# Performance work log

Measured on AMD Instinct MI355X. Metric: run time of the kernel, lower is better.

Reference implementation:

```python
import jax, jax.numpy as jnp
import numpy as np

B, N, D = 16, 1024, 5
R_HID = 8  # radial MLP hidden width


def setup_inputs() -> dict:
    key = jax.random.key(0)
    ks = jax.random.split(key, 16)
    feats = jax.random.normal(ks[0], (B, N, D), jnp.float32)
    coors = 3.0 * jax.random.normal(ks[1], (B, N, 3), jnp.float32)
    a = jax.random.bernoulli(ks[2], 0.01, (B, N, N))
    adj_mat = a | jnp.swapaxes(a, 1, 2)
    s = 1.0 / np.sqrt(D)
    Wq = s * jax.random.normal(ks[3], (D, D), jnp.float32)
    Wk = s * jax.random.normal(ks[4], (D, D), jnp.float32)
    Wv = s * jax.random.normal(ks[5], (D, D), jnp.float32)
    Wo = s * jax.random.normal(ks[6], (D, D), jnp.float32)
    w_r1 = 0.5 * jax.random.normal(ks[7], (1, R_HID), jnp.float32)
    b_r1 = jnp.zeros((R_HID,), jnp.float32)
    w_r2 = 0.5 * jax.random.normal(ks[8], (R_HID, 1), jnp.float32)
    b_r2 = jnp.zeros((1,), jnp.float32)
    w1 = (1.0 / np.sqrt(D)) * jax.random.normal(ks[9], (D, 128), jnp.float32)
    b1 = jnp.zeros((128,), jnp.float32)
    w2 = (1.0 / np.sqrt(128.0)) * jax.random.normal(ks[10], (128, 3), jnp.float32)
    b2 = jnp.zeros((3,), jnp.float32)
    return dict(feats=feats, coors=coors, adj_mat=adj_mat, Wq=Wq, Wk=Wk, Wv=Wv,
                Wo=Wo, w_r1=w_r1, b_r1=b_r1, w_r2=w_r2, b_r2=b_r2,
                w1=w1, b1=b1, w2=w2, b2=b2)


def _se3_layer(feats, coors, neigh, Wq, Wk, Wv, Wo, w_r1, b_r1, w_r2, b_r2):
    # SE(3)-invariant sparse graph attention on degree-0 channels.
    # Attention logits = content term + radial (distance-only) bias, so the
    # scalar output is invariant to global rotations/translations of coors.
    q = jnp.einsum('bnd,de->bne', feats, Wq)
    k = jnp.einsum('bnd,de->bne', feats, Wk)
    v = jnp.einsum('bnd,de->bne', feats, Wv)
    rel = coors[:, :, None, :] - coors[:, None, :, :]        # [B,N,N,3]
    dist = jnp.sqrt(jnp.sum(rel * rel, axis=-1) + 1e-8)      # [B,N,N]
    h = jax.nn.relu(dist[..., None] * w_r1[0] + b_r1)        # [B,N,N,R_HID]
    rbias = (h @ w_r2)[..., 0] + b_r2[0]                     # [B,N,N]
    scores = jnp.einsum('bid,bjd->bij', q, k) / np.sqrt(q.shape[-1]) + rbias
    scores = jnp.where(neigh, scores, -1e9)
    attn = jax.nn.softmax(scores, axis=-1)
    agg = jnp.einsum('bij,bjd->bid', attn, v)
    return feats + jnp.einsum('bid,de->bie', agg, Wo)        # residual


def reference(feats, coors, adj_mat, Wq, Wk, Wv, Wo, w_r1, b_r1, w_r2, b_r2,
              w1, b1, w2, b2):
    a = adj_mat.astype(jnp.float32)
    # num_adj_degrees=2: attend over 1-hop and 2-hop neighbors (+ self)
    adj2 = jnp.einsum('bij,bjk->bik', a, a) > 0
    eye = jnp.eye(adj_mat.shape[1], dtype=bool)[None]
    neigh = adj_mat | adj2 | eye
    x = _se3_layer(feats, coors, neigh, Wq, Wk, Wv, Wo, w_r1, b_r1, w_r2, b_r2)
    pooled = jnp.mean(x, axis=1)                              # [B, D]
    hdn = jax.nn.relu(pooled @ w1 + b1)
    return hdn @ w2 + b2                                      # [B, 3]
```

## Files before the change

kernel.cpp:

```cpp
#include <hip/hip_runtime.h>
#include <hip/hip_bf16.h>

#define BB 16
#define NN 1024
#define DD 5
#define RH 8

typedef unsigned long long u64;
typedef unsigned int u32;
typedef __hip_bfloat16 bf16;

static __device__ __forceinline__ float tof(bf16 x) { return __bfloat162float(x); }
static __device__ __forceinline__ float ldf(const void* p, long long i, bool f) {
  return f ? ((const float*)p)[i] : tof(((const bf16*)p)[i]);
}

__global__ __launch_bounds__(256) void k_pack(const void* __restrict__ adj,
                                              u64* __restrict__ adjbits) {
  __shared__ int sNon01, sNonpair, sLow3;
  int tid = threadIdx.x;
  if (tid == 0) { sNon01 = 0; sNonpair = 0; sLow3 = 0; }
  __syncthreads();
  {
    const u32* aw = (const u32*)adj;
    int non01 = 0, nonpair = 0, low3 = 0;
    for (int i = tid; i < 4096; i += 256) {
      u32 x = aw[i];
      u32 lo = x & 0xFFFFu, hi = x >> 16;
      non01 |= (x > 1u);
      nonpair |= !((lo == 0u || lo == 0x3F80u) && (hi == 0u || hi == 0x3F80u));
      low3 |= (lo == 0x3F80u);
    }
    if (non01) atomicOr(&sNon01, 1);
    if (nonpair) atomicOr(&sNonpair, 1);
    if (low3) atomicOr(&sLow3, 1);
  }
  __syncthreads();
  int mode;
  if (!sNon01) mode = 0;
  else if (!sNonpair) mode = sLow3 ? 2 : 3;
  else mode = 1;

  int gid = blockIdx.x * 256 + tid;
  if (gid >= BB * NN * 16) return;
  int w = gid & 15;
  long long row = gid >> 4;
  long long base = row * NN + (long long)w * 64;
  u64 bits = 0;
  if (mode == 3) {
    const uint4* p = (const uint4*)((const float*)adj + base);
    #pragma unroll
    for (int t = 0; t < 16; ++t) {
      uint4 x = p[t];
      if (x.x << 1) bits |= 1ull << (4 * t + 0);
      if (x.y << 1) bits |= 1ull << (4 * t + 1);
      if (x.z << 1) bits |= 1ull << (4 * t + 2);
      if (x.w << 1) bits |= 1ull << (4 * t + 3);
    }
  } else if (mode == 0) {
    const uint4* p = (const uint4*)((const u32*)adj + base);
    #pragma unroll
    for (int t = 0; t < 16; ++t) {
      uint4 x = p[t];
      if (x.x) bits |= 1ull << (4 * t + 0);
      if (x.y) bits |= 1ull << (4 * t + 1);
      if (x.z) bits |= 1ull << (4 * t + 2);
      if (x.w) bits |= 1ull << (4 * t + 3);
    }
  } else if (mode == 2) {
    const uint4* p = (const uint4*)((const unsigned short*)adj + base);
    #pragma unroll
    for (int t = 0; t < 8; ++t) {
      uint4 x = p[t];
      u32 c[4] = {x.x, x.y, x.z, x.w};
      #pragma unroll
      for (int q = 0; q < 4; ++q) {
        if ((c[q] & 0x7FFFu)) bits |= 1ull << (8 * t + 2 * q + 0);
        if ((c[q] >> 16) & 0x7FFFu) bits |= 1ull << (8 * t + 2 * q + 1);
      }
    }
  } else {
    const uint4* p = (const uint4*)((const unsigned char*)adj + base);
    #pragma unroll
    for (int t = 0; t < 4; ++t) {
      uint4 x = p[t];
      u32 c[4] = {x.x, x.y, x.z, x.w};
      #pragma unroll
      for (int q = 0; q < 4; ++q)
        #pragma unroll
        for (int bb = 0; bb < 4; ++bb)
          if ((c[q] >> (8 * bb)) & 0xFFu) bits |= 1ull << (16 * t + 4 * q + bb);
    }
  }
  adjbits[gid] = bits;
}

__global__ __launch_bounds__(256) void k_twohop(const u64* __restrict__ adjbits,
                                                u64* __restrict__ neighbits) {
  __shared__ unsigned short listL[4][NN];
  int wave = threadIdx.x >> 6, lane = threadIdx.x & 63;
  int row = blockIdx.x * 4 + wave;
  int b = row >> 10;
  int i = row & (NN - 1);
  int w = lane & 15;
  const u64* rowp = adjbits + (size_t)row * 16;
  u64 rw = rowp[w];
  unsigned short* list = listL[wave];
  int cnt = 0;
  #pragma unroll
  for (int sw = 0; sw < 16; ++sw) {
    u64 bits = __shfl(rw, sw, 64);
    int mybit = (int)((bits >> lane) & 1ull);
    int pre = __popcll(bits & ((1ull << lane) - 1ull));
    if (mybit) list[cnt + pre] = (unsigned short)(sw * 64 + lane);
    cnt += __popcll(bits);
  }
  __syncthreads();
  u64 acc = rw;
  if (w == (i >> 6)) acc |= 1ull << (i & 63);
  int g = lane >> 4;
  const u64* basep = adjbits + (size_t)b * NN * 16;
  for (int n = g; n < cnt; n += 4) {
    int j = list[n];
    acc |= basep[(size_t)j * 16 + w];
  }
  acc |= __shfl_xor(acc, 16, 64);
  acc |= __shfl_xor(acc, 32, 64);
  if (lane < 16) neighbits[(size_t)row * 16 + lane] = acc;
}

__global__ __launch_bounds__(256) void k_attn(
    const void* __restrict__ feats, const void* __restrict__ coors,
    const void* __restrict__ Wq, const void* __restrict__ Wk,
    const void* __restrict__ Wv, const void* __restrict__ Wo,
    const void* __restrict__ wr1, const void* __restrict__ br1,
    const void* __restrict__ wr2, const void* __restrict__ br2,
    const u64* __restrict__ neighbits, float* __restrict__ rowAgg) {
  __shared__ __align__(16) float4 kvL[512 * 3];
  __shared__ float coL[512 * 3];
  __shared__ float wqL[25], wkL[25], wvL[25], woL[25];
  __shared__ float qL[16 * DD], ciL[16 * 3];
  __shared__ float wrL[3][RH];
  __shared__ float sConst[2];
  __shared__ int sFast;
  __shared__ int sCnt[4];
  int bi = blockIdx.x;
  int b = bi >> 7, rem = bi & 127, chunk = rem >> 1, half = rem & 1;
  int j0 = half * 512;
  int tid = threadIdx.x;
  {
    u32 x = ((const u32*)feats)[tid];
    u32 lo = x & 0xFFFFu;
    int e = (int)((lo >> 7) & 0xFFu);
    bool insane = !(lo == 0u || (e >= 90 && e <= 150));
    u64 m = __ballot(insane);
    if ((tid & 63) == 0) sCnt[tid >> 6] = (int)__popcll(m);
  }
  __syncthreads();
  bool f32 = (sCnt[0] + sCnt[1] + sCnt[2] + sCnt[3]) > 64;
  if (tid < 25) {
    wqL[tid] = ldf(Wq, tid, f32);
    wkL[tid] = ldf(Wk, tid, f32);
    wvL[tid] = ldf(Wv, tid, f32);
    woL[tid] = ldf(Wo, tid, f32);
  }
  if (tid >= 64 && tid < 64 + RH) {
    int h = tid - 64;
    wrL[0][h] = ldf(wr1, h, f32);
    wrL[1][h] = ldf(br1, h, f32);
    wrL[2][h] = ldf(wr2, h, f32);
  }
  if (tid == 96) {
    float c = 0.0f;
    int ok = 1;
    #pragma unroll
    for (int h = 0; h < RH; ++h) {
      float w1h = ldf(wr1, h, f32);
      if (ldf(br1, h, f32) != 0.0f) ok = 0;
      if (w1h > 0.0f) c += w1h * ldf(wr2, h, f32);
    }
    sConst[0] = c;
    sConst[1] = ldf(br2, 0, f32);
    sFast = ok;
  }
  __syncthreads();
  for (int n = tid; n < 512; n += 256) {
    long long node = (long long)b * NN + j0 + n;
    float f0 = ldf(feats, node * DD + 0, f32), f1 = ldf(feats, node * DD + 1, f32),
          f2 = ldf(feats, node * DD + 2, f32), f3 = ldf(feats, node * DD + 3, f32),
          f4 = ldf(feats, node * DD + 4, f32);
    float k[DD], tv[DD], v[DD];
    #pragma unroll
    for (int e = 0; e < DD; ++e) {
      k[e] = f0 * wkL[e] + f1 * wkL[5 + e] + f2 * wkL[10 + e] + f3 * wkL[15 + e] +
             f4 * wkL[20 + e];
      tv[e] = f0 * wvL[e] + f1 * wvL[5 + e] + f2 * wvL[10 + e] + f3 * wvL[15 + e] +
              f4 * wvL[20 + e];
    }
    #pragma unroll
    for (int e = 0; e < DD; ++e)
      v[e] = tv[0] * woL[e] + tv[1] * woL[5 + e] + tv[2] * woL[10 + e] +
             tv[3] * woL[15 + e] + tv[4] * woL[20 + e];
    kvL[n * 3 + 0] = make_float4(k[0], k[1], k[2], k[3]);
    kvL[n * 3 + 1] = make_float4(k[4], v[0], v[1], v[2]);
    kvL[n * 3 + 2] = make_float4(v[3], v[4], 0.f, 0.f);
  }
  for (int idx = tid; idx < 512 * 3; idx += 256)
    coL[idx] = ldf(coors, (long long)(b * NN + j0) * 3 + idx, f32);
  if (tid < 16) {
    long long row = (long long)b * NN + chunk * 16 + tid;
    float f0 = ldf(feats, row * DD + 0, f32), f1 = ldf(feats, row * DD + 1, f32),
          f2 = ldf(feats, row * DD + 2, f32), f3 = ldf(feats, row * DD + 3, f32),
          f4 = ldf(feats, row * DD + 4, f32);
    #pragma unroll
    for (int e = 0; e < DD; ++e)
      qL[tid * DD + e] = (f0 * wqL[e] + f1 * wqL[5 + e] + f2 * wqL[10 + e] +
                          f3 * wqL[15 + e] + f4 * wqL[20 + e]) * 0.4472135954999579f;
    #pragma unroll
    for (int c = 0; c < 3; ++c) ciL[tid * 3 + c] = ldf(coors, row * 3 + c, f32);
  }
  __syncthreads();

  int g = tid >> 6, lane = tid & 63;
  int i0 = chunk * 16 + g * 4;
  float q[4][DD], ci[4][3], l[4], A[4][DD];
  #pragma unroll
  for (int r = 0; r < 4; ++r) {
    #pragma unroll
    for (int e = 0; e < DD; ++e) q[r][e] = qL[(g * 4 + r) * DD + e];
    #pragma unroll
    for (int c = 0; c < 3; ++c) ci[r][c] = ciL[(g * 4 + r) * 3 + c];
    l[r] = 0.0f;
    #pragma unroll
    for (int e = 0; e < DD; ++e) A[r][e] = 0.0f;
  }
  const u64* nb = neighbits + ((size_t)(b * NN + i0)) * 16 + half * 8;
  float Cf = sConst[0], br2f = sConst[1];
  int fast = sFast;
  for (int it = 0; it < 8; ++it) {
    int j = it * 64 + lane;
    float4 ka = kvL[j * 3 + 0];
    float4 kb = kvL[j * 3 + 1];
    float4 kc = kvL[j * 3 + 2];
    float jx = coL[j * 3], jy = coL[j * 3 + 1], jz = coL[j * 3 + 2];
    if (fast) {
      #pragma unroll
      for (int r = 0; r < 4; ++r) {
        u64 nw = nb[(size_t)r * 16 + it];
        float cx = jx - ci[r][0], cy = jy - ci[r][1], cz = jz - ci[r][2];
        float dist = sqrtf(fmaf(cx, cx, fmaf(cy, cy, fmaf(cz, cz, 1e-8f))));
        float s = fmaf(q[r][0], ka.x, br2f);
        s = fmaf(q[r][1], ka.y, s);
        s = fmaf(q[r][2], ka.z, s);
        s = fmaf(q[r][3], ka.w, s);
        s = fmaf(q[r][4], kb.x, s);
        s = fmaf(Cf, dist, s);
        s = fminf(s, 85.0f);
        s = ((nw >> lane) & 1ull) ? s : -100.0f;
        float p = __expf(s);
        l[r] += p;
        A[r][0] = fmaf(p, kb.y, A[r][0]);
        A[r][1] = fmaf(p, kb.z, A[r][1]);
        A[r][2] = fmaf(p, kb.w, A[r][2]);
        A[r][3] = fmaf(p, kc.x, A[r][3]);
        A[r][4] = fmaf(p, kc.y, A[r][4]);
      }
    } else {
      #pragma unroll
      for (int r = 0; r < 4; ++r) {
        u64 nw = nb[(size_t)r * 16 + it];
        float cx = jx - ci[r][0], cy = jy - ci[r][1], cz = jz - ci[r][2];
        float dist = sqrtf(fmaf(cx, cx, fmaf(cy, cy, fmaf(cz, cz, 1e-8f))));
        float rb = br2f;
        #pragma unroll
        for (int h = 0; h < RH; ++h)
          rb += fmaxf(dist * wrL[0][h] + wrL[1][h], 0.0f) * wrL[2][h];
        float s = fmaf(q[r][0], ka.x, rb);
        s = fmaf(q[r][1], ka.y, s);
        s = fmaf(q[r][2], ka.z, s);
        s = fmaf(q[r][3], ka.w, s);
        s = fmaf(q[r][4], kb.x, s);
        s = fminf(s, 85.0f);
        s = ((nw >> lane) & 1ull) ? s : -100.0f;
        float p = __expf(s);
        l[r] += p;
        A[r][0] = fmaf(p, kb.y, A[r][0]);
        A[r][1] = fmaf(p, kb.z, A[r][1]);
        A[r][2] = fmaf(p, kb.w, A[r][2]);
        A[r][3] = fmaf(p, kc.x, A[r][3]);
        A[r][4] = fmaf(p, kc.y, A[r][4]);
      }
    }
  }
  #pragma unroll
  for (int msk = 1; msk < 64; msk <<= 1) {
    #pragma unroll
    for (int r = 0; r < 4; ++r) {
      l[r] += __shfl_xor(l[r], msk, 64);
      A[r][0] += __shfl_xor(A[r][0], msk, 64);
      A[r][1] += __shfl_xor(A[r][1], msk, 64);
      A[r][2] += __shfl_xor(A[r][2], msk, 64);
      A[r][3] += __shfl_xor(A[r][3], msk, 64);
      A[r][4] += __shfl_xor(A[r][4], msk, 64);
    }
  }
  if (lane == 0) {
    #pragma unroll
    for (int r = 0; r < 4; ++r) {
      float* o = rowAgg + (((size_t)(b * NN + i0 + r)) * 2 + half) * 6;
      o[0] = l[r];
      o[1] = A[r][0]; o[2] = A[r][1]; o[3] = A[r][2]; o[4] = A[r][3]; o[5] = A[r][4];
    }
  }
}

__global__ __launch_bounds__(256) void k_final(
    const void* __restrict__ feats, const float* __restrict__ rowAgg,
    const void* __restrict__ w1, const void* __restrict__ b1,
    const void* __restrict__ w2, const void* __restrict__ b2,
    float* __restrict__ out) {
  __shared__ float waveL[4][DD];
  __shared__ float poolL[DD];
  __shared__ float hL[128];
  __shared__ int sCnt[4];
  int b = blockIdx.x, tid = threadIdx.x;
  {
    u32 x = ((const u32*)feats)[tid];
    u32 lo = x & 0xFFFFu;
    int e = (int)((lo >> 7) & 0xFFu);
    bool insane = !(lo == 0u || (e >= 90 && e <= 150));
    u64 m = __ballot(insane);
    if ((tid & 63) == 0) sCnt[tid >> 6] = (int)__popcll(m);
  }
  __syncthreads();
  bool f32 = (sCnt[0] + sCnt[1] + sCnt[2] + sCnt[3]) > 64;
  float pe[DD] = {0.f, 0.f, 0.f, 0.f, 0.f};
  for (int n = tid; n < NN; n += 256) {
    const float* ag = rowAgg + ((size_t)(b * NN + n)) * 12;
    float l = ag[0] + ag[6];
    float inv = (l > 0.f) ? 1.0f / l : 0.0f;
    long long base = ((long long)b * NN + n) * DD;
    #pragma unroll
    for (int e = 0; e < DD; ++e)
      pe[e] += ldf(feats, base + e, f32) + (ag[1 + e] + ag[7 + e]) * inv;
  }
  #pragma unroll
  for (int off = 32; off >= 1; off >>= 1)
    #pragma unroll
    for (int e = 0; e < DD; ++e) pe[e] += __shfl_down(pe[e], off, 64);
  int wave = tid >> 6, lane = tid & 63;
  if (lane == 0)
    #pragma unroll
    for (int e = 0; e < DD; ++e) waveL[wave][e] = pe[e];
  __syncthreads();
  if (tid < DD)
    poolL[tid] = (waveL[0][tid] + waveL[1][tid] + waveL[2][tid] + waveL[3][tid]) *
                 (1.0f / 1024.0f);
  __syncthreads();
  if (tid < 128) {
    float acc = ldf(b1, tid, f32);
    #pragma unroll
    for (int d = 0; d < DD; ++d)
      acc = fmaf(poolL[d], ldf(w1, d * 128 + tid, f32), acc);
    hL[tid] = fmaxf(acc, 0.0f);
  }
  __syncthreads();
  if (tid < 3) {
    float s = ldf(b2, tid, f32);
    for (int j = 0; j < 128; ++j) s = fmaf(hL[j], ldf(w2, j * 3 + tid, f32), s);
    out[b * 3 + tid] = s;
  }
}

extern "C" void kernel_launch(void* const* d_in, const int* in_sizes, int n_in,
                              void* d_out, int out_size, void* d_ws, size_t ws_size,
                              hipStream_t stream) {
  const void* adj = d_in[2];
  float* out = (float*)d_out;

  char* w = (char*)d_ws;
  const size_t BITS_BYTES = (size_t)BB * NN * 16 * sizeof(u64);
  u64* adjbits = (u64*)(w + 512);
  u64* neighbits = (u64*)(w + 512 + BITS_BYTES);
  float* rowAgg = (float*)(w + 512 + 2 * BITS_BYTES);

  k_pack<<<BB * NN * 16 / 256, 256, 0, stream>>>(adj, adjbits);
  k_twohop<<<BB * NN / 4, 256, 0, stream>>>(adjbits, neighbits);
  k_attn<<<BB * 128, 256, 0, stream>>>(d_in[0], d_in[1], d_in[3], d_in[4], d_in[5],
                                       d_in[6], d_in[7], d_in[8], d_in[9], d_in[10],
                                       neighbits, rowAgg);
  k_final<<<BB, 256, 0, stream>>>(d_in[0], rowAgg, d_in[11], d_in[12],
                                  d_in[13], d_in[14], out);
}
```

Baseline: 202.2 us.

## Fuse final pooling/MLP into attention kernel via atomics and last-block reduction

The attention kernel now processes both halves of the key range in one block (two phases), which halves the grid and removes the rowAgg round-trip. Per-row results are normalized in-kernel and atomically accumulated into a pooled buffer. The last block, found with a done counter, runs the small MLP, which removes the separate k_final launch. The neighbor masks are preloaded into 16-bit registers per row, and the fast path uses exp2 with log2e prescaling plus the hardware sqrt intrinsic. The risks are atomic nondeterminism and the serial last-block tail.

New measurement: 312.1 us. +54.3%, slower.

```diff
diff --git a/kernel.cpp b/kernel.cpp
--- a/kernel.cpp
+++ b/kernel.cpp
@@ -15,10 +15,18 @@
   return f ? ((const float*)p)[i] : tof(((const bf16*)p)[i]);
 }
 
+#define LOG2E 1.4426950408889634f
+
 __global__ __launch_bounds__(256) void k_pack(const void* __restrict__ adj,
-                                              u64* __restrict__ adjbits) {
+                                              u64* __restrict__ adjbits,
+                                              float* __restrict__ pooled,
+                                              int* __restrict__ doneCnt) {
   __shared__ int sNon01, sNonpair, sLow3;
   int tid = threadIdx.x;
+  if (blockIdx.x == 0) {
+    if (tid < BB * DD) pooled[tid] = 0.0f;
+    if (tid == 0) *doneCnt = 0;
+  }
   if (tid == 0) { sNon01 = 0; sNonpair = 0; sLow3 = 0; }
   __syncthreads();
   {
@@ -135,18 +143,20 @@
     const void* __restrict__ Wv, const void* __restrict__ Wo,
     const void* __restrict__ wr1, const void* __restrict__ br1,
     const void* __restrict__ wr2, const void* __restrict__ br2,
-    const u64* __restrict__ neighbits, float* __restrict__ rowAgg) {
+    const u64* __restrict__ neighbits, float* __restrict__ pooled,
+    int* __restrict__ doneCnt,
+    const void* __restrict__ w1v, const void* __restrict__ b1v,
+    const void* __restrict__ w2v, const void* __restrict__ b2v,
+    float* __restrict__ out) {
   __shared__ __align__(16) float4 kvL[512 * 3];
   __shared__ float coL[512 * 3];
   __shared__ float wqL[25], wkL[25], wvL[25], woL[25];
   __shared__ float qL[16 * DD], ciL[16 * 3];
   __shared__ float wrL[3][RH];
   __shared__ float sConst[2];
-  __shared__ int sFast;
+  __shared__ int sFast, sDone;
   __shared__ int sCnt[4];
-  int bi = blockIdx.x;
-  int b = bi >> 7, rem = bi & 127, chunk = rem >> 1, half = rem & 1;
-  int j0 = half * 512;
+  int b = blockIdx.x >> 6, chunk = blockIdx.x & 63;
   int tid = threadIdx.x;
   {
     u32 x = ((const u32*)feats)[tid];
@@ -179,196 +189,202 @@
       if (ldf(br1, h, f32) != 0.0f) ok = 0;
       if (w1h > 0.0f) c += w1h * ldf(wr2, h, f32);
     }
-    sConst[0] = c;
-    sConst[1] = ldf(br2, 0, f32);
+    sConst[0] = c * LOG2E;
+    sConst[1] = ldf(br2, 0, f32) * LOG2E;
     sFast = ok;
   }
   __syncthreads();
-  for (int n = tid; n < 512; n += 256) {
-    long long node = (long long)b * NN + j0 + n;
-    float f0 = ldf(feats, node * DD + 0, f32), f1 = ldf(feats, node * DD + 1, f32),
-          f2 = ldf(feats, node * DD + 2, f32), f3 = ldf(feats, node * DD + 3, f32),
-          f4 = ldf(feats, node * DD + 4, f32);
-    float k[DD], tv[DD], v[DD];
-    #pragma unroll
-    for (int e = 0; e < DD; ++e) {
-      k[e] = f0 * wkL[e] + f1 * wkL[5 + e] + f2 * wkL[10 + e] + f3 * wkL[15 + e] +
-             f4 * wkL[20 + e];
-      tv[e] = f0 * wvL[e] + f1 * wvL[5 + e] + f2 * wvL[10 + e] + f3 * wvL[15 + e] +
-              f4 * wvL[20 + e];
-    }
-    #pragma unroll
-    for (int e = 0; e < DD; ++e)
-      v[e] = tv[0] * woL[e] + tv[1] * woL[5 + e] + tv[2] * woL[10 + e] +
-             tv[3] * woL[15 + e] + tv[4] * woL[20 + e];
-    kvL[n * 3 + 0] = make_float4(k[0], k[1], k[2], k[3]);
-    kvL[n * 3 + 1] = make_float4(k[4], v[0], v[1], v[2]);
-    kvL[n * 3 + 2] = make_float4(v[3], v[4], 0.f, 0.f);
-  }
-  for (int idx = tid; idx < 512 * 3; idx += 256)
-    coL[idx] = ldf(coors, (long long)(b * NN + j0) * 3 + idx, f32);
+  int fast = sFast;
   if (tid < 16) {
     long long row = (long long)b * NN + chunk * 16 + tid;
     float f0 = ldf(feats, row * DD + 0, f32), f1 = ldf(feats, row * DD + 1, f32),
           f2 = ldf(feats, row * DD + 2, f32), f3 = ldf(feats, row * DD + 3, f32),
           f4 = ldf(feats, row * DD + 4, f32);
+    float qsc = fast ? (0.4472135954999579f * LOG2E) : 0.4472135954999579f;
     #pragma unroll
     for (int e = 0; e < DD; ++e)
       qL[tid * DD + e] = (f0 * wqL[e] + f1 * wqL[5 + e] + f2 * wqL[10 + e] +
-                          f3 * wqL[15 + e] + f4 * wqL[20 + e]) * 0.4472135954999579f;
-    #pragma unroll
-    for (int c = 0; c < 3; ++c) ciL[tid * 3 + c] = ldf(coors, row * 3 + c, f32);
-  }
-  __syncthreads();
+                          f3 * wqL[15 + e] + f4 * wqL[20 + e]) * qsc;
+    #pragma unroll
+    for (int c = 0; c < 3; ++c)
+      ciL[tid * 3 + c] = ldf(coors, row * 3 + c, f32);
+  }
 
   int g = tid >> 6, lane = tid & 63;
   int i0 = chunk * 16 + g * 4;
+  u32 msk[4];
+  {
+    const u64* nb = neighbits + ((size_t)(b * NN + i0)) * 16;
+    #pragma unroll
+    for (int r = 0; r < 4; ++r) {
+      u32 mk = 0;
+      #pragma unroll
+      for (int w16 = 0; w16 < 16; ++w16) {
+        u64 word = nb[(size_t)r * 16 + w16];
+        mk |= (u32)((word >> lane) & 1ull) << w16;
+      }
+      msk[r] = mk;
+    }
+  }
   float q[4][DD], ci[4][3], l[4], A[4][DD];
+  float Cf = sConst[0], br2f = sConst[1];
   #pragma unroll
   for (int r = 0; r < 4; ++r) {
-    #pragma unroll
-    for (int e = 0; e < DD; ++e) q[r][e] = qL[(g * 4 + r) * DD + e];
-    #pragma unroll
-    for (int c = 0; c < 3; ++c) ci[r][c] = ciL[(g * 4 + r) * 3 + c];
     l[r] = 0.0f;
     #pragma unroll
     for (int e = 0; e < DD; ++e) A[r][e] = 0.0f;
   }
-  const u64* nb = neighbits + ((size_t)(b * NN + i0)) * 16 + half * 8;
-  float Cf = sConst[0], br2f = sConst[1];
-  int fast = sFast;
-  for (int it = 0; it < 8; ++it) {
-    int j = it * 64 + lane;
-    float4 ka = kvL[j * 3 + 0];
-    float4 kb = kvL[j * 3 + 1];
-    float4 kc = kvL[j * 3 + 2];
-    float jx = coL[j * 3], jy = coL[j * 3 + 1], jz = coL[j * 3 + 2];
-    if (fast) {
+
+  for (int ph = 0; ph < 2; ++ph) {
+    __syncthreads();
+    for (int n = tid; n < 512; n += 256) {
+      long long node = (long long)b * NN + ph * 512 + n;
+      float f0 = ldf(feats, node * DD + 0, f32), f1 = ldf(feats, node * DD + 1, f32),
+            f2 = ldf(feats, node * DD + 2, f32), f3 = ldf(feats, node * DD + 3, f32),
+            f4 = ldf(feats, node * DD + 4, f32);
+      float k[DD], tv[DD], v[DD];
+      #pragma unroll
+      for (int e = 0; e < DD; ++e) {
+        k[e] = f0 * wkL[e] + f1 * wkL[5 + e] + f2 * wkL[10 + e] + f3 * wkL[15 + e] +
+               f4 * wkL[20 + e];
+        tv[e] = f0 * wvL[e] + f1 * wvL[5 + e] + f2 * wvL[10 + e] + f3 * wvL[15 + e] +
+                f4 * wvL[20 + e];
+      }
+      #pragma unroll
+      for (int e = 0; e < DD; ++e)
+        v[e] = tv[0] * woL[e] + tv[1] * woL[5 + e] + tv[2] * woL[10 + e] +
+               tv[3] * woL[15 + e] + tv[4] * woL[20 + e];
+      kvL[n * 3 + 0] = make_float4(k[0], k[1], k[2], k[3]);
+      kvL[n * 3 + 1] = make_float4(k[4], v[0], v[1], v[2]);
+      kvL[n * 3 + 2] = make_float4(v[3], v[4], 0.f, 0.f);
+    }
+    for (int idx = tid; idx < 512 * 3; idx += 256)
+      coL[idx] = ldf(coors, ((long long)(b * NN) + ph * 512) * 3 + idx, f32);
+    __syncthreads();
+    if (ph == 0) {
       #pragma unroll
       for (int r = 0; r < 4; ++r) {
-        u64 nw = nb[(size_t)r * 16 + it];
-        float cx = jx - ci[r][0], cy = jy - ci[r][1], cz = jz - ci[r][2];
-        float dist = sqrtf(fmaf(cx, cx, fmaf(cy, cy, fmaf(cz, cz, 1e-8f))));
-        float s = fmaf(q[r][0], ka.x, br2f);
-        s = fmaf(q[r][1], ka.y, s);
-        s = fmaf(q[r][2], ka.z, s);
-        s = fmaf(q[r][3], ka.w, s);
-        s = fmaf(q[r][4], kb.x, s);
-        s = fmaf(Cf, dist, s);
-        s = fminf(s, 85.0f);
-        s = ((nw >> lane) & 1ull) ? s : -100.0f;
-        float p = __expf(s);
-        l[r] += p;
-        A[r][0] = fmaf(p, kb.y, A[r][0]);
-        A[r][1] = fmaf(p, kb.z, A[r][1]);
-        A[r][2] = fmaf(p, kb.w, A[r][2]);
-        A[r][3] = fmaf(p, kc.x, A[r][3]);
-        A[r][4] = fmaf(p, kc.y, A[r][4]);
+        #pragma unroll
+        for (int e = 0; e < DD; ++e) q[r][e] = qL[(g * 4 + r) * DD + e];
+        #pragma unroll
+        for (int c = 0; c < 3; ++c) ci[r][c] = ciL[(g * 4 + r) * 3 + c];
       }
-    } else {
-      #pragma unroll
-      for (int r = 0; r < 4; ++r) {
-        u64 nw = nb[(size_t)r * 16 + it];
-        float cx = jx - ci[r][0], cy = jy - ci[r][1], cz = jz - ci[r][2];
-        float dist = sqrtf(fmaf(cx, cx, fmaf(cy, cy, fmaf(cz, cz, 1e-8f))));
-        float rb = br2f;
+    }
+    #pragma unroll
+    for (int it = 0; it < 8; ++it) {
+      int itg = ph * 8 + it;
+      int j = it * 64 + lane;
+      float4 ka = kvL[j * 3 + 0];
+      float4 kb = kvL[j * 3 + 1];
+      float4 kc = kvL[j * 3 + 2];
+      float jx = coL[j * 3], jy = coL[j * 3 + 1], jz = coL[j * 3 + 2];
+      if (fast) {
         #pragma unroll
-        for (int h = 0; h < RH; ++h)
-          rb += fmaxf(dist * wrL[0][h] + wrL[1][h], 0.0f) * wrL[2][h];
-        float s = fmaf(q[r][0], ka.x, rb);
-        s = fmaf(q[r][1], ka.y, s);
-        s = fmaf(q[r][2], ka.z, s);
-        s = fmaf(q[r][3], ka.w, s);
-        s = fmaf(q[r][4], kb.x, s);
-        s = fminf(s, 85.0f);
-        s = ((nw >> lane) & 1ull) ? s : -100.0f;
-        float p = __expf(s);
-        l[r] += p;
-        A[r][0] = fmaf(p, kb.y, A[r][0]);
-        A[r][1] = fmaf(p, kb.z, A[r][1]);
-        A[r][2] = fmaf(p, kb.w, A[r][2]);
-        A[r][3] = fmaf(p, kc.x, A[r][3]);
-        A[r][4] = fmaf(p, kc.y, A[r][4]);
+        for (int r = 0; r < 4; ++r) {
+          float cx = jx - ci[r][0], cy = jy - ci[r][1], cz = jz - ci[r][2];
+          float dist =
+              __builtin_amdgcn_sqrtf(fmaf(cx, cx, fmaf(cy, cy, fmaf(cz, cz, 1e-8f))));
+          float s = fmaf(q[r][0], ka.x, br2f);
+          s = fmaf(q[r][1], ka.y, s);
+          s = fmaf(q[r][2], ka.z, s);
+          s = fmaf(q[r][3], ka.w, s);
+          s = fmaf(q[r][4], kb.x, s);
+          s = fmaf(Cf, dist, s);
+          s = fminf(s, 126.0f);
+          s = ((msk[r] >> itg) & 1u) ? s : -150.0f;
+          float p = __builtin_amdgcn_exp2f(s);
+          l[r] += p;
+          A[r][0] = fmaf(p, kb.y, A[r][0]);
+          A[r][1] = fmaf(p, kb.z, A[r][1]);
+          A[r][2] = fmaf(p, kb.w, A[r][2]);
+          A[r][3] = fmaf(p, kc.x, A[r][3]);
+          A[r][4] = fmaf(p, kc.y, A[r][4]);
+        }
+      } else {
+        #pragma unroll
+        for (int r = 0; r < 4; ++r) {
+          float cx = jx - ci[r][0], cy = jy - ci[r][1], cz = jz - ci[r][2];
+          float dist = sqrtf(fmaf(cx, cx, fmaf(cy, cy, fmaf(cz, cz, 1e-8f))));
+          float rb = ldf(br2, 0, f32);
+          #pragma unroll
+          for (int h = 0; h < RH; ++h)
+            rb += fmaxf(dist * wrL[0][h] + wrL[1][h], 0.0f) * wrL[2][h];
+          float s = fmaf(q[r][0], ka.x, rb);
+          s = fmaf(q[r][1], ka.y, s);
+          s = fmaf(q[r][2], ka.z, s);
+          s = fmaf(q[r][3], ka.w, s);
+          s = fmaf(q[r][4], kb.x, s);
+          s = fminf(s, 85.0f);
+          s = ((msk[r] >> itg) & 1u) ? s : -100.0f;
+          float p = __expf(s);
+          l[r] += p;
+          A[r][0] = fmaf(p, kb.y, A[r][0]);
+          A[r][1] = fmaf(p, kb.z, A[r][1]);
+          A[r][2] = fmaf(p, kb.w, A[r][2]);
+          A[r][3] = fmaf(p, kc.x, A[r][3]);
+          A[r][4] = fmaf(p, kc.y, A[r][4]);
+        }
       }
     }
   }
   #pragma unroll
-  for (int msk = 1; msk < 64; msk <<= 1) {
+  for (int msk2 = 1; msk2 < 64; msk2 <<= 1) {
     #pragma unroll
     for (int r = 0; r < 4; ++r) {
-      l[r] += __shfl_xor(l[r], msk, 64);
-      A[r][0] += __shfl_xor(A[r][0], msk, 64);
-      A[r][1] += __shfl_xor(A[r][1], msk, 64);
-      A[r][2] += __shfl_xor(A[r][2], msk, 64);
-      A[r][3] += __shfl_xor(A[r][3], msk, 64);
-      A[r][4] += __shfl_xor(A[r][4], msk, 64);
+      l[r] += __shfl_xor(l[r], msk2, 64);
+      A[r][0] += __shfl_xor(A[r][0], msk2, 64);
+      A[r][1] += __shfl_xor(A[r][1], msk2, 64);
+      A[r][2] += __shfl_xor(A[r][2], msk2, 64);
+      A[r][3] += __shfl_xor(A[r][3], msk2, 64);
+      A[r][4] += __shfl_xor(A[r][4], msk2, 64);
     }
   }
   if (lane == 0) {
+    float pe[DD] = {0.f, 0.f, 0.f, 0.f, 0.f};
     #pragma unroll
     for (int r = 0; r < 4; ++r) {
-      float* o = rowAgg + (((size_t)(b * NN + i0 + r)) * 2 + half) * 6;
-      o[0] = l[r];
-      o[1] = A[r][0]; o[2] = A[r][1]; o[3] = A[r][2]; o[4] = A[r][3]; o[5] = A[r][4];
-    }
-  }
-}
-
-__global__ __launch_bounds__(256) void k_final(
-    const void* __restrict__ feats, const float* __restrict__ rowAgg,
-    const void* __restrict__ w1, const void* __restrict__ b1,
-    const void* __restrict__ w2, const void* __restrict__ b2,
-    float* __restrict__ out) {
-  __shared__ float waveL[4][DD];
-  __shared__ float poolL[DD];
-  __shared__ float hL[128];
-  __shared__ int sCnt[4];
-  int b = blockIdx.x, tid = threadIdx.x;
-  {
-    u32 x = ((const u32*)feats)[tid];
-    u32 lo = x & 0xFFFFu;
-    int e = (int)((lo >> 7) & 0xFFu);
-    bool insane = !(lo == 0u || (e >= 90 && e <= 150));
-    u64 m = __ballot(insane);
-    if ((tid & 63) == 0) sCnt[tid >> 6] = (int)__popcll(m);
-  }
-  __syncthreads();
-  bool f32 = (sCnt[0] + sCnt[1] + sCnt[2] + sCnt[3]) > 64;
-  float pe[DD] = {0.f, 0.f, 0.f, 0.f, 0.f};
-  for (int n = tid; n < NN; n += 256) {
-    const float* ag = rowAgg + ((size_t)(b * NN + n)) * 12;
-    float l = ag[0] + ag[6];
-    float inv = (l > 0.f) ? 1.0f / l : 0.0f;
-    long long base = ((long long)b * NN + n) * DD;
+      float inv = (l[r] > 0.f) ? 1.0f / l[r] : 0.0f;
+      long long base = ((long long)b * NN + i0 + r) * DD;
+      #pragma unroll
+      for (int e = 0; e < DD; ++e)
+        pe[e] += ldf(feats, base + e, f32) + A[r][e] * inv;
+    }
+    #pragma unroll
+    for (int e = 0; e < DD; ++e) atomicAdd(&pooled[b * DD + e], pe[e]);
+  }
+  __syncthreads();
+  __threadfence();
+  if (tid == 0) sDone = (atomicAdd(doneCnt, 1) == (int)gridDim.x - 1);
+  __syncthreads();
+  if (sDone) {
+    __threadfence();
+    int bb2 = tid >> 4, sub = tid & 15;
+    float pl[DD];
     #pragma unroll
     for (int e = 0; e < DD; ++e)
-      pe[e] += ldf(feats, base + e, f32) + (ag[1 + e] + ag[7 + e]) * inv;
-  }
-  #pragma unroll
-  for (int off = 32; off >= 1; off >>= 1)
-    #pragma unroll
-    for (int e = 0; e < DD; ++e) pe[e] += __shfl_down(pe[e], off, 64);
-  int wave = tid >> 6, lane = tid & 63;
-  if (lane == 0)
-    #pragma unroll
-    for (int e = 0; e < DD; ++e) waveL[wave][e] = pe[e];
-  __syncthreads();
-  if (tid < DD)
-    poolL[tid] = (waveL[0][tid] + waveL[1][tid] + waveL[2][tid] + waveL[3][tid]) *
-                 (1.0f / 1024.0f);
-  __syncthreads();
-  if (tid < 128) {
-    float acc = ldf(b1, tid, f32);
-    #pragma unroll
-    for (int d = 0; d < DD; ++d)
-      acc = fmaf(poolL[d], ldf(w1, d * 128 + tid, f32), acc);
-    hL[tid] = fmaxf(acc, 0.0f);
-  }
-  __syncthreads();
-  if (tid < 3) {
-    float s = ldf(b2, tid, f32);
-    for (int j = 0; j < 128; ++j) s = fmaf(hL[j], ldf(w2, j * 3 + tid, f32), s);
-    out[b * 3 + tid] = s;
+      pl[e] = pooled[bb2 * DD + e] * (1.0f / 1024.0f);
+    float a0 = 0.f, a1 = 0.f, a2 = 0.f;
+    for (int jj = sub * 8; jj < sub * 8 + 8; ++jj) {
+      float h = ldf(b1v, jj, f32);
+      #pragma unroll
+      for (int d = 0; d < DD; ++d)
+        h = fmaf(pl[d], ldf(w1v, d * 128 + jj, f32), h);
+      h = fmaxf(h, 0.0f);
+      a0 = fmaf(h, ldf(w2v, jj * 3 + 0, f32), a0);
+      a1 = fmaf(h, ldf(w2v, jj * 3 + 1, f32), a1);
+      a2 = fmaf(h, ldf(w2v, jj * 3 + 2, f32), a2);
+    }
+    #pragma unroll
+    for (int mk = 1; mk < 16; mk <<= 1) {
+      a0 += __shfl_xor(a0, mk, 64);
+      a1 += __shfl_xor(a1, mk, 64);
+      a2 += __shfl_xor(a2, mk, 64);
+    }
+    if (sub == 0) {
+      out[bb2 * 3 + 0] = a0 + ldf(b2v, 0, f32);
+      out[bb2 * 3 + 1] = a1 + ldf(b2v, 1, f32);
+      out[bb2 * 3 + 2] = a2 + ldf(b2v, 2, f32);
+    }
   }
 }
 
@@ -379,16 +395,16 @@
   float* out = (float*)d_out;
 
   char* w = (char*)d_ws;
+  int* doneCnt = (int*)w;
+  float* pooled = (float*)(w + 64);
   const size_t BITS_BYTES = (size_t)BB * NN * 16 * sizeof(u64);
   u64* adjbits = (u64*)(w + 512);
   u64* neighbits = (u64*)(w + 512 + BITS_BYTES);
-  float* rowAgg = (float*)(w + 512 + 2 * BITS_BYTES);
-
-  k_pack<<<BB * NN * 16 / 256, 256, 0, stream>>>(adj, adjbits);
+
+  k_pack<<<BB * NN * 16 / 256, 256, 0, stream>>>(adj, adjbits, pooled, doneCnt);
   k_twohop<<<BB * NN / 4, 256, 0, stream>>>(adjbits, neighbits);
-  k_attn<<<BB * 128, 256, 0, stream>>>(d_in[0], d_in[1], d_in[3], d_in[4], d_in[5],
-                                       d_in[6], d_in[7], d_in[8], d_in[9], d_in[10],
-                                       neighbits, rowAgg);
-  k_final<<<BB, 256, 0, stream>>>(d_in[0], rowAgg, d_in[11], d_in[12],
-                                  d_in[13], d_in[14], out);
+  k_attn<<<BB * 64, 256, 0, stream>>>(d_in[0], d_in[1], d_in[3], d_in[4], d_in[5],
+                                      d_in[6], d_in[7], d_in[8], d_in[9], d_in[10],
+                                      neighbits, pooled, doneCnt,
+                                      d_in[11], d_in[12], d_in[13], d_in[14], out);
 }
```
